# Kernel tuning notes

Measured on AMD Instinct MI355X. Metric: run time of the kernel, lower is better.

## Reference

```python
import jax, jax.numpy as jnp
import numpy as np

TEMPERATURE = 0.5
TAU_PLUS = 0.1
EPS = 1e-8


def setup_inputs() -> dict:
    key = jax.random.key(0)
    k1, k2 = jax.random.split(key)
    B, D = 8192, 128
    z_i = jax.random.normal(k1, (B, D), dtype=jnp.float32)
    z_j = jax.random.normal(k2, (B, D), dtype=jnp.float32)
    return {"z_i": z_i, "z_j": z_j}


def _l2_normalize(x, axis=1, eps=1e-12):
    # matches torch F.normalize: x / max(||x||, eps)
    n = jnp.linalg.norm(x, axis=axis, keepdims=True)
    return x / jnp.maximum(n, eps)


def reference(z_i, z_j):
    B = z_i.shape[0]
    zi = _l2_normalize(z_i, axis=1)
    zj = _l2_normalize(z_j, axis=1)
    reps = jnp.concatenate([zi, zj], axis=0)  # [2B, D]
    sim = jnp.matmul(reps, reps.T) / TEMPERATURE  # [2B, 2B]
    sim = sim - jnp.max(sim, axis=1, keepdims=True)
    mask = jnp.eye(2 * B, dtype=bool)
    sim = jnp.where(mask, -9e15, sim)
    pos = jnp.exp(jnp.sum(zi * zj, axis=-1) / TEMPERATURE)  # [B]
    positives = jnp.concatenate([pos, pos], axis=0)  # [2B]
    neg_sum = jnp.sum(jnp.exp(sim), axis=1)  # [2B]
    Ng = (-TAU_PLUS * B * positives + neg_sum) / (1.0 - TAU_PLUS)
    Ng = jnp.maximum(Ng, B * jnp.exp(jnp.asarray(-1.0 / TEMPERATURE, dtype=sim.dtype)))
    loss = -jnp.log(positives / (positives + Ng + EPS))
    return jnp.mean(loss)
```

## Files before the change

### kernel.cpp

```cpp
#include <hip/hip_runtime.h>
#include <hip/hip_bf16.h>

typedef __attribute__((ext_vector_type(8))) short bf16x8;
typedef __attribute__((ext_vector_type(4))) float f32x4;

#define B_ROWS 8192
#define NROWS 16384
#define D 128
#define C1 2.8853900817779268f
#define E_M2 0.13533528323661270f
#define RSCALE 1.6986436f
#define TILE_COLS 128
#define TILE_BYTES (TILE_COLS * D * 2)
#define NSPLIT 16
#define NBLK (64 * NSPLIT)
#define NSLICE 8

__device__ __forceinline__ float fast_exp2(float x) {
#if __has_builtin(__builtin_amdgcn_exp2f)
    return __builtin_amdgcn_exp2f(x);
#else
    float r; asm("v_exp_f32 %0, %1" : "=v"(r) : "v"(x)); return r;
#endif
}
__device__ __forceinline__ float fast_log2(float x) {
#if __has_builtin(__builtin_amdgcn_logf)
    return __builtin_amdgcn_logf(x);
#else
    float r; asm("v_log_f32 %0, %1" : "=v"(r) : "v"(x)); return r;
#endif
}

__device__ __forceinline__ unsigned short f2bf(float f) {
    union { float f; unsigned u; } v; v.f = f;
    unsigned r = v.u + 0x7FFFu + ((v.u >> 16) & 1u);
    return (unsigned short)(r >> 16);
}

__device__ __host__ __forceinline__ int colpart_off(int I) {
    return I * NROWS - 128 * I * (I + 1);
}

__global__ __launch_bounds__(256) void k_norm(const float* __restrict__ zi,
                                              const float* __restrict__ zj,
                                              unsigned* __restrict__ repsU,
                                              float* __restrict__ pos) {
    int w = threadIdx.x >> 6, lane = threadIdx.x & 63;
    int row = blockIdx.x * 4 + w;
    const float2* a2 = (const float2*)(zi + (size_t)row * D);
    const float2* b2 = (const float2*)(zj + (size_t)row * D);
    float2 a = a2[lane], b = b2[lane];
    float si = a.x * a.x + a.y * a.y;
    float sj = b.x * b.x + b.y * b.y;
    float sd = a.x * b.x + a.y * b.y;
#pragma unroll
    for (int m = 32; m; m >>= 1) {
        si += __shfl_xor(si, m);
        sj += __shfl_xor(sj, m);
        sd += __shfl_xor(sd, m);
    }
    float inv_i = 1.0f / fmaxf(sqrtf(si), 1e-12f);
    float inv_j = 1.0f / fmaxf(sqrtf(sj), 1e-12f);
    float sa = inv_i * RSCALE, sb = inv_j * RSCALE;
    repsU[(size_t)row * 64 + lane] =
        (unsigned)f2bf(a.x * sa) | ((unsigned)f2bf(a.y * sa) << 16);
    repsU[(size_t)(row + B_ROWS) * 64 + lane] =
        (unsigned)f2bf(b.x * sb) | ((unsigned)f2bf(b.y * sb) << 16);
    if (lane == 0) pos[row] = fast_exp2(sd * inv_i * inv_j * C1);
}

__global__ __launch_bounds__(256, 2) void k_negsum(const unsigned short* __restrict__ R,
                                                   float* __restrict__ rowpart,
                                                   float* __restrict__ colpart) {
    __shared__ char smem[2][TILE_BYTES];
    __shared__ float colacc[2][16][16][8];
    int I = blockIdx.x >> 4;
    int s = blockIdx.x & (NSPLIT - 1);
    int rowBase = I << 8;
    int j0 = I << 1;
    int dph = (s - (j0 & 15)) & 15;
    int jstart = j0 + dph;
    int nt = (jstart < 128) ? (((127 - jstart) >> 4) + 1) : 0;

    int w = threadIdx.x >> 6;
    int lane = threadIdx.x & 63;
    int lr = lane & 15, lk = lane >> 4;
    int waveRow = rowBase + (w << 6);

    bf16x8 afrag[4][4];
#pragma unroll
    for (int r = 0; r < 4; ++r)
#pragma unroll
        for (int kk = 0; kk < 4; ++kk)
            afrag[r][kk] = *(const bf16x8*)(R + (size_t)(waveRow + r * 16 + lr) * D + kk * 32 + lk * 8);

    int srcoff[8], dstoff[8];
#pragma unroll
    for (int j = 0; j < 8; ++j) {
        int o = (w * 8 + j) * 1024 + lane * 16;
        int row = o >> 8, c = o & 255;
        srcoff[j] = row * 256 + (c ^ ((row & 7) << 4));
        dstoff[j] = (w * 8 + j) * 1024;
    }

    const char* Rb = (const char*)R;

    int m64 = (lr & 4) << 4;
    int lbase = lr * 256 + ((lk * 16) ^ ((lr & 3) << 4));

    float acc[4][4] = {};

#define STAGE(buf, jj)                                                            \
    do {                                                                          \
        const char* tb_ = Rb + (size_t)(jj) * TILE_BYTES;                         \
        _Pragma("unroll")                                                         \
        for (int j = 0; j < 8; ++j)                                               \
            __builtin_amdgcn_global_load_lds(                                     \
                (const __attribute__((address_space(1))) unsigned*)(tb_ + srcoff[j]), \
                (__attribute__((address_space(3))) unsigned*)(&smem[buf][dstoff[j]]), \
                16, 0, 0);                                                        \
    } while (0)

#define BATCH_BODY(DIAG)                                                          \
    do {                                                                          \
        _Pragma("unroll")                                                         \
        for (int ct = 0; ct < 8; ++ct) {                                          \
            const char* cb_ = sb + ct * 4096;                                     \
            bf16x8 b0 = *(const bf16x8*)(cb_ + (0 ^ m64));                        \
            bf16x8 b1 = *(const bf16x8*)(cb_ + (64 ^ m64));                       \
            bf16x8 b2 = *(const bf16x8*)(cb_ + (128 ^ m64));                      \
            bf16x8 b3 = *(const bf16x8*)(cb_ + (192 ^ m64));                      \
            _Pragma("unroll")                                                     \
            for (int r = 0; r < 4; ++r) {                                         \
                f32x4 c = {0.f, 0.f, 0.f, 0.f};                                   \
                c = __builtin_amdgcn_mfma_f32_16x16x32_bf16(afrag[r][0], b0, c, 0, 0, 0); \
                c = __builtin_amdgcn_mfma_f32_16x16x32_bf16(afrag[r][1], b1, c, 0, 0, 0); \
                c = __builtin_amdgcn_mfma_f32_16x16x32_bf16(afrag[r][2], b2, c, 0, 0, 0); \
                c = __builtin_amdgcn_mfma_f32_16x16x32_bf16(afrag[r][3], b3, c, 0, 0, 0); \
                if (DIAG && ct == ctd + r) {                                      \
                    _Pragma("unroll")                                             \
                    for (int q = 0; q < 4; ++q)                                   \
                        if (lk * 4 + q != lr) {                                   \
                            float e = fast_exp2(c[q]);                            \
                            acc[r][q] += e; csum[ct] += e;                        \
                        }                                                         \
                } else {                                                          \
                    _Pragma("unroll")                                             \
                    for (int q = 0; q < 4; ++q) {                                 \
                        float e = fast_exp2(c[q]);                                \
                        acc[r][q] += e; csum[ct] += e;                            \
                    }                                                             \
                }                                                                 \
            }                                                                     \
        }                                                                         \
    } while (0)

    if (nt > 0) STAGE(0, jstart);
    __syncthreads();
    int cur = 0;
    for (int t = 0; t < nt; ++t) {
        int jt = jstart + (t << 4);
        int colBase = jt << 7;
        if (t > 0 && w == ((t + 3) & 3)) {
            int pcb = colBase - 2048;
            if (pcb >= rowBase + 256) {
                int par = (t - 1) & 1;
                float v0 = 0.f, v1 = 0.f;
#pragma unroll
                for (int u = 0; u < 16; ++u) {
                    v0 += colacc[par][u][lane & 15][lane >> 4];
                    v1 += colacc[par][u][lane & 15][4 + (lane >> 4)];
                }
                int cb = colpart_off(I) + pcb - ((I + 1) << 8);
                colpart[cb + lane] = v0;
                colpart[cb + 64 + lane] = v1;
            }
        }
        if (t + 1 < nt) STAGE(cur ^ 1, jt + 16);
        const char* sb = &smem[cur][0] + lbase;
        float csum[8] = {};
        bool dg = (unsigned)(waveRow - colBase) < 128u;
        int ctd = (waveRow - colBase) >> 4;
        if (dg) {
            BATCH_BODY(true);
        } else {
            BATCH_BODY(false);
        }
        bool offdiag = (colBase >= rowBase + 256);
        if (offdiag) {
            int par = t & 1;
            f32x4 cs0 = {csum[0], csum[1], csum[2], csum[3]};
            f32x4 cs1 = {csum[4], csum[5], csum[6], csum[7]};
            *(f32x4*)&colacc[par][(w << 2) | lk][lr][0] = cs0;
            *(f32x4*)&colacc[par][(w << 2) | lk][lr][4] = cs1;
        }
        __syncthreads();
        cur ^= 1;
    }
    if (nt > 0 && w == ((nt + 3) & 3)) {
        int pcb = (jstart + ((nt - 1) << 4)) << 7;
        if (pcb >= rowBase + 256) {
            int par = (nt - 1) & 1;
            float v0 = 0.f, v1 = 0.f;
#pragma unroll
            for (int u = 0; u < 16; ++u) {
                v0 += colacc[par][u][lane & 15][lane >> 4];
                v1 += colacc[par][u][lane & 15][4 + (lane >> 4)];
            }
            int cb = colpart_off(I) + pcb - ((I + 1) << 8);
            colpart[cb + lane] = v0;
            colpart[cb + 64 + lane] = v1;
        }
    }
#undef STAGE
#undef BATCH_BODY

#pragma unroll
    for (int r = 0; r < 4; ++r)
#pragma unroll
        for (int q = 0; q < 4; ++q) {
            float v = acc[r][q];
            v += __shfl_xor(v, 1);
            v += __shfl_xor(v, 2);
            v += __shfl_xor(v, 4);
            v += __shfl_xor(v, 8);
            if (lr == 0)
                rowpart[(size_t)s * NROWS + waveRow + r * 16 + lk * 4 + q] = v;
        }
}

__global__ __launch_bounds__(256) void k_negred(const float* __restrict__ rowpart,
                                                const float* __restrict__ colpart,
                                                float* __restrict__ negp) {
    int g = blockIdx.x >> 3;
    int z = blockIdx.x & (NSLICE - 1);
    int i = g * 256 + threadIdx.x;
    float a = 0.f;
#pragma unroll
    for (int s = z; s < NSPLIT; s += NSLICE)
        a += rowpart[(size_t)s * NROWS + i];
    for (int I = z; I < g; I += NSLICE)
        a += colpart[colpart_off(I) + i - ((I + 1) << 8)];
    negp[(size_t)z * NROWS + i] = a;
}

__global__ __launch_bounds__(256) void k_loss1(const float* __restrict__ pos,
                                               const float* __restrict__ negp,
                                               float* __restrict__ bsum) {
    int i = blockIdx.x * 256 + threadIdx.x;
    float neg = 0.f;
#pragma unroll
    for (int z = 0; z < NSLICE; ++z) neg += negp[(size_t)z * NROWS + i];
    neg *= E_M2;
    float p = pos[i & (B_ROWS - 1)];
    float Ng = fmaxf((neg - 819.2f * p) * (1.0f / 0.9f), 8192.0f * E_M2);
    float l = fast_log2((p + Ng + 1e-8f) / p) * 0.69314718056f;
#pragma unroll
    for (int m = 32; m; m >>= 1) l += __shfl_xor(l, m);
    __shared__ float s4[4];
    int wv = threadIdx.x >> 6;
    if ((threadIdx.x & 63) == 0) s4[wv] = l;
    __syncthreads();
    if (threadIdx.x == 0) bsum[blockIdx.x] = s4[0] + s4[1] + s4[2] + s4[3];
}

__global__ void k_loss2(const float* __restrict__ bsum, float* __restrict__ out) {
    float v = bsum[threadIdx.x];
#pragma unroll
    for (int m = 32; m; m >>= 1) v += __shfl_xor(v, m);
    if (threadIdx.x == 0) out[0] = v * (1.0f / (float)NROWS);
}

extern "C" void kernel_launch(void* const* d_in, const int* in_sizes, int n_in,
                              void* d_out, int out_size, void* d_ws, size_t ws_size,
                              hipStream_t stream) {
    const float* zi = (const float*)d_in[0];
    const float* zj = (const float*)d_in[1];
    char* ws = (char*)d_ws;
    unsigned short* reps = (unsigned short*)ws;
    float* pos = (float*)(ws + 4194304);
    float* rowpart = pos + B_ROWS;
    float* colpart = rowpart + (size_t)NSPLIT * NROWS;
    float* negp = colpart + 516096;
    float* bsum = negp + (size_t)NSLICE * NROWS;
    float* out = (float*)d_out;

    k_norm<<<B_ROWS / 4, 256, 0, stream>>>(zi, zj, (unsigned*)reps, pos);
    k_negsum<<<NBLK, 256, 0, stream>>>(reps, rowpart, colpart);
    k_negred<<<64 * NSLICE, 256, 0, stream>>>(rowpart, colpart, negp);
    k_loss1<<<NROWS / 256, 256, 0, stream>>>(pos, negp, bsum);
    k_loss2<<<1, 64, 0, stream>>>(bsum, out);
}
```

Before: 66.36 us.

## Split tile staging into halves with counted vmcnt waits and priority hints

The column-tile loop now stages each next tile in two halves, each issued right after a barrier, instead of one full tile behind a full __syncthreads. Explicit s_waitcnt vmcnt(4) lets computation on the current half start while the other half is still in flight. The per-wave LDS chunk assignment is interleaved so each half is spread across all waves, and s_setprio raises priority around the MFMA sections. Loads past the end are clamped to the last tile, so some tiles are loaded redundantly, and correctness now depends on the hand-counted vmcnt values.

```diff
diff --git a/kernel.cpp b/kernel.cpp
--- a/kernel.cpp
+++ b/kernel.cpp
@@ -97,10 +97,10 @@
     int srcoff[8], dstoff[8];
 #pragma unroll
     for (int j = 0; j < 8; ++j) {
-        int o = (w * 8 + j) * 1024 + lane * 16;
+        int o = (j * 4 + w) * 1024 + lane * 16;
         int row = o >> 8, c = o & 255;
         srcoff[j] = row * 256 + (c ^ ((row & 7) << 4));
-        dstoff[j] = (w * 8 + j) * 1024;
+        dstoff[j] = (j * 4 + w) * 1024;
     }
 
     const char* Rb = (const char*)R;
@@ -110,21 +110,23 @@
 
     float acc[4][4] = {};
 
-#define STAGE(buf, jj)                                                            \
+#define STAGE_HALF(v, h)                                                          \
     do {                                                                          \
-        const char* tb_ = Rb + (size_t)(jj) * TILE_BYTES;                         \
+        int vc_ = (v) < nt ? (v) : nt - 1;                                        \
+        char* dbase_ = &smem[(v) & 1][0];                                         \
+        const char* tb_ = Rb + (size_t)(jstart + (vc_ << 4)) * TILE_BYTES;        \
         _Pragma("unroll")                                                         \
-        for (int j = 0; j < 8; ++j)                                               \
+        for (int j = (h) * 4; j < (h) * 4 + 4; ++j)                               \
             __builtin_amdgcn_global_load_lds(                                     \
                 (const __attribute__((address_space(1))) unsigned*)(tb_ + srcoff[j]), \
-                (__attribute__((address_space(3))) unsigned*)(&smem[buf][dstoff[j]]), \
+                (__attribute__((address_space(3))) unsigned*)(dbase_ + dstoff[j]), \
                 16, 0, 0);                                                        \
     } while (0)
 
-#define BATCH_BODY(DIAG)                                                          \
+#define BATCH_HALF(H, DIAG)                                                       \
     do {                                                                          \
         _Pragma("unroll")                                                         \
-        for (int ct = 0; ct < 8; ++ct) {                                          \
+        for (int ct = (H) * 4; ct < (H) * 4 + 4; ++ct) {                          \
             const char* cb_ = sb + ct * 4096;                                     \
             bf16x8 b0 = *(const bf16x8*)(cb_ + (0 ^ m64));                        \
             bf16x8 b1 = *(const bf16x8*)(cb_ + (64 ^ m64));                       \
@@ -155,16 +157,60 @@
         }                                                                         \
     } while (0)
 
-    if (nt > 0) STAGE(0, jstart);
-    __syncthreads();
-    int cur = 0;
-    for (int t = 0; t < nt; ++t) {
-        int jt = jstart + (t << 4);
-        int colBase = jt << 7;
-        if (t > 0 && w == ((t + 3) & 3)) {
-            int pcb = colBase - 2048;
+    if (nt > 0) {
+        STAGE_HALF(0, 0);
+        STAGE_HALF(0, 1);
+        for (int t = 0; t < nt; ++t) {
+            int jt = jstart + (t << 4);
+            int colBase = jt << 7;
+            const char* sb = &smem[t & 1][0] + lbase;
+            float csum[8] = {};
+            bool dg = (unsigned)(waveRow - colBase) < 128u;
+            int ctd = (waveRow - colBase) >> 4;
+
+            asm volatile("s_waitcnt vmcnt(4) lgkmcnt(0)" ::: "memory");
+            __builtin_amdgcn_s_barrier();
+            STAGE_HALF(t + 1, 0);
+            if (t > 0 && w == ((t + 3) & 3)) {
+                int pcb = colBase - 2048;
+                if (pcb >= rowBase + 256) {
+                    int par = (t - 1) & 1;
+                    float v0 = 0.f, v1 = 0.f;
+#pragma unroll
+                    for (int u = 0; u < 16; ++u) {
+                        v0 += colacc[par][u][lane & 15][lane >> 4];
+                        v1 += colacc[par][u][lane & 15][4 + (lane >> 4)];
+                    }
+                    int cb = colpart_off(I) + pcb - ((I + 1) << 8);
+                    colpart[cb + lane] = v0;
+                    colpart[cb + 64 + lane] = v1;
+                }
+            }
+            __builtin_amdgcn_s_setprio(1);
+            if (dg) { BATCH_HALF(0, true); } else { BATCH_HALF(0, false); }
+            __builtin_amdgcn_s_setprio(0);
+
+            asm volatile("s_waitcnt vmcnt(4) lgkmcnt(0)" ::: "memory");
+            __builtin_amdgcn_s_barrier();
+            STAGE_HALF(t + 1, 1);
+            __builtin_amdgcn_s_setprio(1);
+            if (dg) { BATCH_HALF(1, true); } else { BATCH_HALF(1, false); }
+            __builtin_amdgcn_s_setprio(0);
+
+            bool offdiag = (colBase >= rowBase + 256);
+            if (offdiag) {
+                int par = t & 1;
+                f32x4 cs0 = {csum[0], csum[1], csum[2], csum[3]};
+                f32x4 cs1 = {csum[4], csum[5], csum[6], csum[7]};
+                *(f32x4*)&colacc[par][(w << 2) | lk][lr][0] = cs0;
+                *(f32x4*)&colacc[par][(w << 2) | lk][lr][4] = cs1;
+            }
+        }
+        __syncthreads();
+        if (w == ((nt + 3) & 3)) {
+            int pcb = (jstart + ((nt - 1) << 4)) << 7;
             if (pcb >= rowBase + 256) {
-                int par = (t - 1) & 1;
+                int par = (nt - 1) & 1;
                 float v0 = 0.f, v1 = 0.f;
 #pragma unroll
                 for (int u = 0; u < 16; ++u) {
@@ -176,44 +222,9 @@
                 colpart[cb + 64 + lane] = v1;
             }
         }
-        if (t + 1 < nt) STAGE(cur ^ 1, jt + 16);
-        const char* sb = &smem[cur][0] + lbase;
-        float csum[8] = {};
-        bool dg = (unsigned)(waveRow - colBase) < 128u;
-        int ctd = (waveRow - colBase) >> 4;
-        if (dg) {
-            BATCH_BODY(true);
-        } else {
-            BATCH_BODY(false);
-        }
-        bool offdiag = (colBase >= rowBase + 256);
-        if (offdiag) {
-            int par = t & 1;
-            f32x4 cs0 = {csum[0], csum[1], csum[2], csum[3]};
-            f32x4 cs1 = {csum[4], csum[5], csum[6], csum[7]};
-            *(f32x4*)&colacc[par][(w << 2) | lk][lr][0] = cs0;
-            *(f32x4*)&colacc[par][(w << 2) | lk][lr][4] = cs1;
-        }
-        __syncthreads();
-        cur ^= 1;
     }
-    if (nt > 0 && w == ((nt + 3) & 3)) {
-        int pcb = (jstart + ((nt - 1) << 4)) << 7;
-        if (pcb >= rowBase + 256) {
-            int par = (nt - 1) & 1;
-            float v0 = 0.f, v1 = 0.f;
-#pragma unroll
-            for (int u = 0; u < 16; ++u) {
-                v0 += colacc[par][u][lane & 15][lane >> 4];
-                v1 += colacc[par][u][lane & 15][4 + (lane >> 4)];
-            }
-            int cb = colpart_off(I) + pcb - ((I + 1) << 8);
-            colpart[cb + lane] = v0;
-            colpart[cb + 64 + lane] = v1;
-        }
-    }
-#undef STAGE
-#undef BATCH_BODY
+#undef STAGE_HALF
+#undef BATCH_HALF
 
 #pragma unroll
     for (int r = 0; r < 4; ++r)
```

Result: slower. 72.72 us (+9.6%).
